# Optimization experiments

Measured on AMD Instinct MI355X. Metric: run time of the kernel, lower is better.

## Reference

```python
import jax, jax.numpy as jnp
import numpy as np

DIM = 2048
N_HEADS = 16
HEAD_DIM = DIM // N_HEADS  # 128
HIDDEN = 8192
EPS = 1e-6
NEG = -1e9


def rmsnorm(x, w):
    xf = x.astype(jnp.float32)
    y = xf * jax.lax.rsqrt(jnp.mean(xf * xf, axis=-1, keepdims=True) + EPS)
    return y.astype(x.dtype) * w


def apply_rope(x, cos, sin):
    # x: [B,S,H,Hd]; cos/sin: [S,Hd//2] -> broadcast [1,S,1,Hd//2]
    xf = x.astype(jnp.float32)
    xr = xf[..., 0::2]
    xi = xf[..., 1::2]
    c = cos[None, :, None, :]
    s = sin[None, :, None, :]
    or_ = xr * c - xi * s
    oi_ = xr * s + xi * c
    out = jnp.stack([or_, oi_], axis=-1).reshape(x.shape)
    return out.astype(x.dtype)


def setup_inputs() -> dict:
    key = jax.random.key(0)
    ks = jax.random.split(key, 10)
    B, S = 1, 2048
    x = jax.random.normal(ks[0], (B, S, DIM), dtype=jnp.float32)
    # RoPE frequencies (Llama-style, theta=10000)
    inv_freq = 1.0 / (10000.0 ** (jnp.arange(0, HEAD_DIM, 2, dtype=jnp.float32) / HEAD_DIM))
    angles = jnp.arange(S, dtype=jnp.float32)[:, None] * inv_freq[None, :]  # [S, Hd//2]
    freqs_cos = jnp.cos(angles)
    freqs_sin = jnp.sin(angles)
    # causal additive mask [1,1,S,S]
    mask = jnp.where(jnp.tril(jnp.ones((S, S), dtype=bool)), 0.0, NEG).astype(jnp.float32)[None, None]
    sc = 0.02
    wq = jax.random.normal(ks[1], (DIM, DIM), dtype=jnp.float32) * sc
    wk = jax.random.normal(ks[2], (DIM, DIM), dtype=jnp.float32) * sc
    wv = jax.random.normal(ks[3], (DIM, DIM), dtype=jnp.float32) * sc
    wo = jax.random.normal(ks[4], (DIM, DIM), dtype=jnp.float32) * sc
    w1 = jax.random.normal(ks[5], (DIM, HIDDEN), dtype=jnp.float32) * sc
    w2 = jax.random.normal(ks[6], (HIDDEN, DIM), dtype=jnp.float32) * sc
    w3 = jax.random.normal(ks[7], (DIM, HIDDEN), dtype=jnp.float32) * sc
    attn_norm_w = jnp.ones((DIM,), dtype=jnp.float32)
    ffn_norm_w = jnp.ones((DIM,), dtype=jnp.float32)
    return {"x": x, "freqs_cos": freqs_cos, "freqs_sin": freqs_sin, "mask": mask,
            "wq": wq, "wk": wk, "wv": wv, "wo": wo, "w1": w1, "w2": w2, "w3": w3,
            "attn_norm_w": attn_norm_w, "ffn_norm_w": ffn_norm_w}


def reference(x, freqs_cos, freqs_sin, mask, wq, wk, wv, wo, w1, w2, w3, attn_norm_w, ffn_norm_w):
    B, S, D = x.shape
    # --- attention (pre-norm) ---
    hn = rmsnorm(x, attn_norm_w)
    q = (hn @ wq).reshape(B, S, N_HEADS, HEAD_DIM)
    k = (hn @ wk).reshape(B, S, N_HEADS, HEAD_DIM)
    v = (hn @ wv).reshape(B, S, N_HEADS, HEAD_DIM)
    q = apply_rope(q, freqs_cos, freqs_sin)
    k = apply_rope(k, freqs_cos, freqs_sin)
    scores = jnp.einsum('bqhd,bkhd->bhqk', q, k) / (HEAD_DIM ** 0.5) + mask
    attn = jax.nn.softmax(scores.astype(jnp.float32), axis=-1).astype(q.dtype)
    ctx = jnp.einsum('bhqk,bkhd->bqhd', attn, v).reshape(B, S, D)
    h = x + ctx @ wo
    # --- SwiGLU FFN (pre-norm) ---
    fn = rmsnorm(h, ffn_norm_w)
    ff = (jax.nn.silu(fn @ w1) * (fn @ w3)) @ w2
    return h + ff
```

## Files before the change

### kernel.cpp

```cpp
#include <hip/hip_runtime.h>
#include <hip/hip_bf16.h>

#define DIM 2048
#define HEAD_DIM 128
#define N_HEADS 16
#define SEQ 2048
#define HID 8192
#define SQKV 6144

typedef short bf16x8 __attribute__((ext_vector_type(8)));
typedef float f32x4 __attribute__((ext_vector_type(4)));
using bf16 = __hip_bfloat16;

#define MFMA16(a, b, c) __builtin_amdgcn_mfma_f32_16x16x32_bf16(a, b, c, 0, 0, 0)

__device__ __forceinline__ unsigned short f2bu(float f) {
    union { bf16 b; unsigned short u; } cv;
    cv.b = __float2bfloat16(f);
    return cv.u;
}

__device__ __forceinline__ void gl16(const void* g, void* l) {
    __builtin_amdgcn_global_load_lds(
        (const __attribute__((address_space(1))) unsigned int*)g,
        (__attribute__((address_space(3))) unsigned int*)l, 16, 0, 0);
}

__global__ __launch_bounds__(256) void rmsnorm_bf16_k(
    const float* __restrict__ x, const float* __restrict__ w, bf16* __restrict__ y)
{
    const int row = blockIdx.x;
    const int tid = threadIdx.x;
    const float* xr = x + (size_t)row * DIM;
    float4 v0 = ((const float4*)xr)[tid];
    float4 v1 = ((const float4*)xr)[tid + 256];
    float ss = v0.x*v0.x + v0.y*v0.y + v0.z*v0.z + v0.w*v0.w
             + v1.x*v1.x + v1.y*v1.y + v1.z*v1.z + v1.w*v1.w;
    for (int o = 32; o > 0; o >>= 1) ss += __shfl_down(ss, o);
    __shared__ float red[4];
    if ((tid & 63) == 0) red[tid >> 6] = ss;
    __syncthreads();
    float tot = red[0] + red[1] + red[2] + red[3];
    float r = rsqrtf(tot * (1.0f / DIM) + 1e-6f);
    float4 w0 = ((const float4*)w)[tid];
    float4 w1 = ((const float4*)w)[tid + 256];
    ushort4 o0, o1;
    o0.x = f2bu(v0.x * r * w0.x); o0.y = f2bu(v0.y * r * w0.y);
    o0.z = f2bu(v0.z * r * w0.z); o0.w = f2bu(v0.w * r * w0.w);
    o1.x = f2bu(v1.x * r * w1.x); o1.y = f2bu(v1.y * r * w1.y);
    o1.z = f2bu(v1.z * r * w1.z); o1.w = f2bu(v1.w * r * w1.w);
    ushort4* yr = (ushort4*)(y + (size_t)row * DIM);
    yr[tid] = o0;
    yr[tid + 256] = o1;
}

__global__ __launch_bounds__(256) void rmsnorm4_k(
    const float* __restrict__ part, const float* __restrict__ x,
    const float* __restrict__ w, float* __restrict__ hout, bf16* __restrict__ y)
{
    const int row = blockIdx.x;
    const int tid = threadIdx.x;
    const size_t base = (size_t)row * DIM;
    const size_t SP = (size_t)SEQ * DIM;
    float4 r0, r1;
    float ss = 0.0f;
    {
        float4 a  = ((const float4*)(x + base))[tid];
        float4 p0 = ((const float4*)(part + base))[tid];
        float4 p1 = ((const float4*)(part + SP + base))[tid];
        float4 p2 = ((const float4*)(part + 2 * SP + base))[tid];
        float4 p3 = ((const float4*)(part + 3 * SP + base))[tid];
        r0.x = a.x + ((p0.x + p1.x) + (p2.x + p3.x));
        r0.y = a.y + ((p0.y + p1.y) + (p2.y + p3.y));
        r0.z = a.z + ((p0.z + p1.z) + (p2.z + p3.z));
        r0.w = a.w + ((p0.w + p1.w) + (p2.w + p3.w));
        ((float4*)(hout + base))[tid] = r0;
        ss += r0.x*r0.x + r0.y*r0.y + r0.z*r0.z + r0.w*r0.w;
    }
    {
        const int t2 = tid + 256;
        float4 a  = ((const float4*)(x + base))[t2];
        float4 p0 = ((const float4*)(part + base))[t2];
        float4 p1 = ((const float4*)(part + SP + base))[t2];
        float4 p2 = ((const float4*)(part + 2 * SP + base))[t2];
        float4 p3 = ((const float4*)(part + 3 * SP + base))[t2];
        r1.x = a.x + ((p0.x + p1.x) + (p2.x + p3.x));
        r1.y = a.y + ((p0.y + p1.y) + (p2.y + p3.y));
        r1.z = a.z + ((p0.z + p1.z) + (p2.z + p3.z));
        r1.w = a.w + ((p0.w + p1.w) + (p2.w + p3.w));
        ((float4*)(hout + base))[t2] = r1;
        ss += r1.x*r1.x + r1.y*r1.y + r1.z*r1.z + r1.w*r1.w;
    }
    for (int o = 32; o > 0; o >>= 1) ss += __shfl_down(ss, o);
    __shared__ float red[4];
    if ((tid & 63) == 0) red[tid >> 6] = ss;
    __syncthreads();
    float tot = red[0] + red[1] + red[2] + red[3];
    float r = rsqrtf(tot * (1.0f / DIM) + 1e-6f);
    float4 w0 = ((const float4*)w)[tid];
    float4 w1 = ((const float4*)w)[tid + 256];
    ushort4 o0, o1;
    o0.x = f2bu(r0.x * r * w0.x); o0.y = f2bu(r0.y * r * w0.y);
    o0.z = f2bu(r0.z * r * w0.z); o0.w = f2bu(r0.w * r * w0.w);
    o1.x = f2bu(r1.x * r * w1.x); o1.y = f2bu(r1.y * r * w1.y);
    o1.z = f2bu(r1.z * r * w1.z); o1.w = f2bu(r1.w * r * w1.w);
    ushort4* yr = (ushort4*)(y + base);
    yr[tid] = o0;
    yr[tid + 256] = o1;
}

__global__ __launch_bounds__(256) void reduce4_k(
    const float* __restrict__ part, const float* __restrict__ h, float* __restrict__ out)
{
    const size_t i = (size_t)blockIdx.x * 256 + threadIdx.x;
    const size_t SP4 = (size_t)SEQ * DIM / 4;
    float4 a  = ((const float4*)h)[i];
    float4 p0 = ((const float4*)part)[i];
    float4 p1 = ((const float4*)part)[i + SP4];
    float4 p2 = ((const float4*)part)[i + 2 * SP4];
    float4 p3 = ((const float4*)part)[i + 3 * SP4];
    float4 r;
    r.x = a.x + ((p0.x + p1.x) + (p2.x + p3.x));
    r.y = a.y + ((p0.y + p1.y) + (p2.y + p3.y));
    r.z = a.z + ((p0.z + p1.z) + (p2.z + p3.z));
    r.w = a.w + ((p0.w + p1.w) + (p2.w + p3.w));
    ((float4*)out)[i] = r;
}

__global__ __launch_bounds__(256) void convT_f32_bf16_k(
    const float* __restrict__ in, bf16* __restrict__ out, int R, int C)
{
    __shared__ float t[32][33];
    const int tx = threadIdx.x, ty = threadIdx.y;
    const int x0 = blockIdx.x * 32, y0 = blockIdx.y * 32;
#pragma unroll
    for (int i = 0; i < 4; ++i)
        t[ty + i * 8][tx] = in[(size_t)(y0 + ty + i * 8) * C + x0 + tx];
    __syncthreads();
#pragma unroll
    for (int i = 0; i < 4; ++i)
        out[(size_t)(x0 + ty + i * 8) * R + y0 + tx] = __float2bfloat16(t[tx][ty + i * 8]);
}

__global__ __launch_bounds__(256) void convT3_f32_bf16_k(
    const float* __restrict__ wq, const float* __restrict__ wk,
    const float* __restrict__ wv, bf16* __restrict__ out)
{
    const int z = blockIdx.z;
    const float* in = z == 0 ? wq : (z == 1 ? wk : wv);
    bf16* o = out + (size_t)z * DIM * DIM;
    __shared__ float t[32][33];
    const int tx = threadIdx.x, ty = threadIdx.y;
    const int x0 = blockIdx.x * 32, y0 = blockIdx.y * 32;
#pragma unroll
    for (int i = 0; i < 4; ++i)
        t[ty + i * 8][tx] = in[(size_t)(y0 + ty + i * 8) * DIM + x0 + tx];
    __syncthreads();
#pragma unroll
    for (int i = 0; i < 4; ++i)
        o[(size_t)(x0 + ty + i * 8) * DIM + y0 + tx] = __float2bfloat16(t[tx][ty + i * 8]);
}

__global__ __launch_bounds__(256) void transpose_bf16_k(
    const bf16* __restrict__ in, int istride, bf16* __restrict__ out)
{
    __shared__ unsigned short t[32][33];
    const int tx = threadIdx.x, ty = threadIdx.y;
    const int x = blockIdx.x * 32 + tx;
    const int y0 = blockIdx.y * 32;
    const unsigned short* inu = (const unsigned short*)in;
    unsigned short* outu = (unsigned short*)out;
#pragma unroll
    for (int i = 0; i < 4; ++i)
        t[ty + i * 8][tx] = inu[(size_t)(y0 + ty + i * 8) * istride + x];
    __syncthreads();
    const int x2 = blockIdx.y * 32 + tx;
    const int y2 = blockIdx.x * 32;
#pragma unroll
    for (int i = 0; i < 4; ++i)
        outu[(size_t)(y2 + ty + i * 8) * SEQ + x2] = t[tx][ty + i * 8];
}

__global__ __launch_bounds__(256) void rope_qk_k(
    bf16* __restrict__ q, bf16* __restrict__ k,
    const float* __restrict__ cosb, const float* __restrict__ sinb)
{
    const int gid = blockIdx.x * 256 + threadIdx.x;
    const int s = gid >> 10;
    const int p = gid & 1023;
    const int h = p >> 6, j = p & 63;
    const size_t off = (size_t)s * SQKV + h * HEAD_DIM + 2 * j;
    const float c = cosb[s * 64 + j], sn = sinb[s * 64 + j];
    float xr = __bfloat162float(q[off]), xi = __bfloat162float(q[off + 1]);
    q[off]     = __float2bfloat16(xr * c - xi * sn);
    q[off + 1] = __float2bfloat16(xr * sn + xi * c);
    xr = __bfloat162float(k[off]); xi = __bfloat162float(k[off + 1]);
    k[off]     = __float2bfloat16(xr * c - xi * sn);
    k[off + 1] = __float2bfloat16(xr * sn + xi * c);
}

template <int EP>
__global__ __launch_bounds__(512, 2) void gemm256_k(
    const bf16* __restrict__ A, const bf16* __restrict__ Bt,
    bf16* __restrict__ Cb, const bf16* other, float* __restrict__ Pf,
    int M, int N, int K, int gx, int ntile, int Ks)
{
    extern __shared__ char smem[];
    const int t512 = threadIdx.x;
    const int w = t512 >> 6, lane = t512 & 63;
    const int lr = lane & 15, lg = lane >> 4;
    const int wm = w >> 2, wn = w & 3;
    const int bofs = (wn & 1) * 64;

    const int nwg = gridDim.x;
    const int q8 = nwg >> 3, r8 = nwg & 7;
    const int xcd = blockIdx.x & 7, seqq = blockIdx.x >> 3;
    const int wgid = (xcd < r8 ? xcd * (q8 + 1) : r8 * (q8 + 1) + (xcd - r8) * q8) + seqq;
    const int split = wgid / ntile;
    const int tile = wgid % ntile;
    const int grp = tile / (4 * gx), rem = tile % (4 * gx);
    const int m0 = (grp * 4 + (rem & 3)) * 256, n0 = (rem >> 2) * 256;
    const int kb0 = split * Ks;
    const int nt = Ks >> 6;

    const bf16* aS[2][2]; const bf16* bS[2][2];
    int sOff[2];
#pragma unroll
    for (int c = 0; c < 2; ++c) {
        const int s = (c * 512 + t512) * 16;
        const int pp = s ^ (((s >> 7) & 7) << 4);
        const int row = pp >> 7, colE = (pp & 127) >> 1;
        sOff[c] = s;
#pragma unroll
        for (int hs = 0; hs < 2; ++hs) {
            aS[hs][c] = A  + (size_t)(m0 + hs * 128 + row) * K + kb0 + colE;
            bS[hs][c] = Bt + (size_t)(n0 + hs * 128 + row) * K + kb0 + colE;
        }
    }
    auto stageA = [&](int buf, int kt) {
#pragma unroll
        for (int hs = 0; hs < 2; ++hs) {
            char* base = smem + (buf * 2 + hs) * 16384;
            gl16(aS[hs][0] + (kt << 6), base + sOff[0]);
            gl16(aS[hs][1] + (kt << 6), base + sOff[1]);
        }
    };
    auto stageB = [&](int buf, int kt) {
#pragma unroll
        for (int hs = 0; hs < 2; ++hs) {
            char* base = smem + 65536 + (buf * 2 + hs) * 16384;
            gl16(bS[hs][0] + (kt << 6), base + sOff[0]);
            gl16(bS[hs][1] + (kt << 6), base + sOff[1]);
        }
    };

    f32x4 acc[8][4] = {};
    bf16x8 bfr[4][2];

    stageB(0, 0); stageA(0, 0);
    stageB(1, 1); stageA(1, 1);

#define SB __builtin_amdgcn_sched_barrier(0)
#define WAITL4 SB; asm volatile("s_waitcnt lgkmcnt(4)" ::: "memory"); SB
#define WAITL0 SB; asm volatile("s_waitcnt lgkmcnt(0)" ::: "memory"); SB
#define LDA_(mf, ks, dst) { int off = (((mf) * 16 + lr) * 128) + ((((ks) * 64) + lg * 16) ^ ((lr & 7) << 4)); \
        dst = *(const bf16x8*)(Am + off); }
#define LDB_(nf, ks, dst) { int off = ((bofs + (nf) * 16 + lr) * 128) + ((((ks) * 64) + lg * 16) ^ ((lr & 7) << 4)); \
        dst = *(const bf16x8*)(Bm + off); }
#define MFMA_PH(mf0, r0, r1, r2, r3) { \
        __builtin_amdgcn_s_setprio(1); \
        _Pragma("unroll") \
        for (int nf = 0; nf < 4; ++nf) { \
            acc[(mf0)][nf]     = MFMA16(r0, bfr[nf][0], acc[(mf0)][nf]); \
            acc[(mf0)][nf]     = MFMA16(r1, bfr[nf][1], acc[(mf0)][nf]); \
            acc[(mf0) + 1][nf] = MFMA16(r2, bfr[nf][0], acc[(mf0) + 1][nf]); \
            acc[(mf0) + 1][nf] = MFMA16(r3, bfr[nf][1], acc[(mf0) + 1][nf]); \
        } \
        __builtin_amdgcn_s_setprio(0); }

    for (int t = 0; t < nt; ++t) {
        const int cur = t & 1;
        if (t + 1 < nt) { asm volatile("s_waitcnt vmcnt(8)" ::: "memory"); }
        else            { asm volatile("s_waitcnt vmcnt(0)" ::: "memory"); }
        SB;
        __builtin_amdgcn_s_barrier();

        const char* Am = smem + (cur * 2 + wm) * 16384;
        const char* Bm = smem + 65536 + (cur * 2 + (wn >> 1)) * 16384;
        const bool pf = (t + 2 < nt);

        bf16x8 x0, x1, x2, x3, y0, y1, y2, y3;
#pragma unroll
        for (int nf = 0; nf < 4; ++nf) { LDB_(nf, 0, bfr[nf][0]) LDB_(nf, 1, bfr[nf][1]) }
        LDA_(0, 0, x0) LDA_(0, 1, x1) LDA_(1, 0, x2) LDA_(1, 1, x3)
        SB;
        LDA_(2, 0, y0) LDA_(2, 1, y1) LDA_(3, 0, y2) LDA_(3, 1, y3)
        WAITL4;
        MFMA_PH(0, x0, x1, x2, x3)
        __builtin_amdgcn_s_barrier();
        if (pf) stageB(cur, t + 2);

        LDA_(4, 0, x0) LDA_(4, 1, x1) LDA_(5, 0, x2) LDA_(5, 1, x3)
        WAITL4;
        MFMA_PH(2, y0, y1, y2, y3)

        LDA_(6, 0, y0) LDA_(6, 1, y1) LDA_(7, 0, y2) LDA_(7, 1, y3)
        WAITL4;
        MFMA_PH(4, x0, x1, x2, x3)

        WAITL0;
        MFMA_PH(6, y0, y1, y2, y3)
        __builtin_amdgcn_s_barrier();
        if (pf) stageA(cur, t + 2);
    }
#undef LDA_
#undef LDB_
#undef MFMA_PH
#undef WAITL4
#undef WAITL0
#undef SB

    float* pf_base = Pf + (size_t)split * M * N;
#pragma unroll
    for (int mf = 0; mf < 8; ++mf)
#pragma unroll
        for (int nf = 0; nf < 4; ++nf) {
            const int row = m0 + wm * 128 + mf * 16 + lg * 4;
            const int col = n0 + wn * 64 + nf * 16 + lr;
#pragma unroll
            for (int r = 0; r < 4; ++r) {
                const size_t idx = (size_t)(row + r) * N + col;
                const float v = acc[mf][nf][r];
                if (EP == 0) {
                    Cb[idx] = __float2bfloat16(v);
                } else if (EP == 2) {
                    const float gg = __bfloat162float(other[idx]);
                    const float sg = gg / (1.0f + __expf(-gg));
                    Cb[idx] = __float2bfloat16(sg * v);
                } else {
                    pf_base[idx] = v;
                }
            }
        }
}

__global__ __launch_bounds__(256) void attn_fwd_k(
    const bf16* __restrict__ qkv, const bf16* __restrict__ vT, bf16* __restrict__ ctx)
{
    const int tid = threadIdx.x;
    const int w = tid >> 6, lane = tid & 63;
    const int lr = lane & 15, lg = lane >> 4;
    const int h = blockIdx.y;
    const int qidx = (blockIdx.y < 8) ? blockIdx.x : (31 - blockIdx.x);
    const int q0b = qidx * 64;
    const int nt = qidx + 1;

    __shared__ __align__(16) unsigned short Kt[2][64 * 128];
    __shared__ __align__(16) unsigned short Vt[2][128 * 64];
    __shared__ __align__(16) unsigned short Pp[4][16 * 64];

    const char* kbase = (const char*)(qkv + DIM + h * HEAD_DIM);
    const char* vbase = (const char*)(vT + (size_t)h * HEAD_DIM * SEQ);

    const int krow_c = tid >> 4;
    const int kcolB  = (tid & 15) * 16;
    const int vrow_c = tid >> 3;
    const int vcolB  = (tid & 7) * 16;

    auto stage = [&](int buf, int kb) {
#pragma unroll
        for (int c = 0; c < 4; ++c) {
            const int r = c * 16 + krow_c;
            gl16(kbase + (size_t)(kb + r) * (SQKV * 2) + (kcolB ^ ((r & 7) << 4)),
                 &Kt[buf][c * 2048 + tid * 8]);
        }
#pragma unroll
        for (int c = 0; c < 4; ++c) {
            const int r = c * 32 + vrow_c;
            gl16(vbase + (size_t)r * (SEQ * 2) + kb * 2 + (vcolB ^ ((r & 7) << 4)),
                 &Vt[buf][c * 2048 + tid * 8]);
        }
    };

    bf16x8 qf[4];
    const bf16* qrow = qkv + (size_t)(q0b + w * 16 + lr) * SQKV + h * HEAD_DIM;
#pragma unroll
    for (int dt = 0; dt < 4; ++dt)
        qf[dt] = *(const bf16x8*)(qrow + dt * 32 + lg * 8);

    f32x4 o[8] = {};
    float m[4], l[4];
#pragma unroll
    for (int j = 0; j < 4; ++j) { m[j] = -3e38f; l[j] = 0.0f; }
    const float scale = 0.08838834764831845f;

    stage(0, 0);
    __syncthreads();

    int cur = 0;
    for (int t = 0; t < nt; ++t) {
        const int kb = t * 64;
        if (t + 1 < nt) stage(cur ^ 1, kb + 64);

        f32x4 s[4] = {};
        __builtin_amdgcn_s_setprio(1);
#pragma unroll
        for (int ss = 0; ss < 4; ++ss) {
            const int r = ss * 16 + lr;
            const int sw = (r & 7) << 3;
#pragma unroll
            for (int dt = 0; dt < 4; ++dt) {
                bf16x8 kf = *(const bf16x8*)&Kt[cur][r * 128 + ((dt * 32 + lg * 8) ^ sw)];
                s[ss] = MFMA16(qf[dt], kf, s[ss]);
            }
        }
        __builtin_amdgcn_s_setprio(0);

        float al[4];
#pragma unroll
        for (int j = 0; j < 4; ++j) {
            const int qi = q0b + w * 16 + lg * 4 + j;
            const int prow = lg * 4 + j;
            const int psw = (prow & 7) << 3;
            float a[4];
#pragma unroll
            for (int ss = 0; ss < 4; ++ss)
                a[ss] = s[ss][j] * scale + ((kb + ss * 16 + lr) > qi ? -1e9f : 0.0f);
            float mx = fmaxf(fmaxf(a[0], a[1]), fmaxf(a[2], a[3]));
            mx = fmaxf(mx, __shfl_xor(mx, 1));
            mx = fmaxf(mx, __shfl_xor(mx, 2));
            mx = fmaxf(mx, __shfl_xor(mx, 4));
            mx = fmaxf(mx, __shfl_xor(mx, 8));
            const float mn = fmaxf(m[j], mx);
            const float asc = __expf(m[j] - mn);
            float e0 = __expf(a[0] - mn), e1 = __expf(a[1] - mn);
            float e2 = __expf(a[2] - mn), e3 = __expf(a[3] - mn);
            float rs = (e0 + e1) + (e2 + e3);
            rs += __shfl_xor(rs, 1); rs += __shfl_xor(rs, 2);
            rs += __shfl_xor(rs, 4); rs += __shfl_xor(rs, 8);
            l[j] = l[j] * asc + rs;
            m[j] = mn;
            al[j] = asc;
            Pp[w][prow * 64 + ((lr)      ^ psw)] = f2bu(e0);
            Pp[w][prow * 64 + ((16 + lr) ^ psw)] = f2bu(e1);
            Pp[w][prow * 64 + ((32 + lr) ^ psw)] = f2bu(e2);
            Pp[w][prow * 64 + ((48 + lr) ^ psw)] = f2bu(e3);
        }
#pragma unroll
        for (int d2 = 0; d2 < 8; ++d2)
#pragma unroll
            for (int j = 0; j < 4; ++j) o[d2][j] *= al[j];

        asm volatile("s_waitcnt lgkmcnt(0)" ::: "memory");
        __builtin_amdgcn_sched_barrier(0);
        const int asw = (lr & 7) << 3;
        bf16x8 pa0 = *(const bf16x8*)&Pp[w][lr * 64 + ((lg * 8)      ^ asw)];
        bf16x8 pa1 = *(const bf16x8*)&Pp[w][lr * 64 + ((32 + lg * 8) ^ asw)];

        __builtin_amdgcn_s_setprio(1);
#pragma unroll
        for (int d2 = 0; d2 < 8; ++d2) {
            const int rv = d2 * 16 + lr;
            const int vsw = (rv & 7) << 3;
            bf16x8 vf0 = *(const bf16x8*)&Vt[cur][rv * 64 + ((lg * 8)      ^ vsw)];
            bf16x8 vf1 = *(const bf16x8*)&Vt[cur][rv * 64 + ((32 + lg * 8) ^ vsw)];
            o[d2] = MFMA16(pa0, vf0, o[d2]);
            o[d2] = MFMA16(pa1, vf1, o[d2]);
        }
        __builtin_amdgcn_s_setprio(0);

        __syncthreads();
        cur ^= 1;
    }

#pragma unroll
    for (int j = 0; j < 4; ++j) {
        const float inv = 1.0f / l[j];
        bf16* dst = ctx + (size_t)(q0b + w * 16 + lg * 4 + j) * DIM + h * HEAD_DIM + lr;
#pragma unroll
        for (int d2 = 0; d2 < 8; ++d2)
            dst[d2 * 16] = __float2bfloat16(o[d2][j] * inv);
    }
}

extern "C" void kernel_launch(void* const* d_in, const int* in_sizes, int n_in,
                              void* d_out, int out_size, void* d_ws, size_t ws_size,
                              hipStream_t stream)
{
    const float* x   = (const float*)d_in[0];
    const float* fc  = (const float*)d_in[1];
    const float* fs  = (const float*)d_in[2];
    const float* wq  = (const float*)d_in[4];
    const float* wk  = (const float*)d_in[5];
    const float* wv  = (const float*)d_in[6];
    const float* wo  = (const float*)d_in[7];
    const float* w1  = (const float*)d_in[8];
    const float* w2  = (const float*)d_in[9];
    const float* w3  = (const float*)d_in[10];
    const float* anw = (const float*)d_in[11];
    const float* fnw = (const float*)d_in[12];
    float* out = (float*)d_out;

    char* p = (char*)d_ws;
    auto alloc = [&](size_t n) { char* r = p; p += (n + 255) & ~(size_t)255; return r; };
    bf16* wT  = (bf16*)alloc((size_t)HID * DIM * 2);
    bf16* hn  = (bf16*)alloc((size_t)SEQ * DIM * 2);
    bf16* qkv = (bf16*)alloc((size_t)SEQ * SQKV * 2);
    bf16* vt  = (bf16*)alloc((size_t)SEQ * DIM * 2);
    bf16* ctx = (bf16*)alloc((size_t)SEQ * DIM * 2);
    bf16* fn  = (bf16*)alloc((size_t)SEQ * DIM * 2);
    float* h  = (float*)alloc((size_t)SEQ * DIM * 4);
    bf16* g   = (bf16*)alloc((size_t)SEQ * HID * 2);
    float* sk = (float*)alloc((size_t)4 * SEQ * DIM * 4);

    const dim3 tb32(32, 8);
    const int LDS256 = 131072;
    (void)hipFuncSetAttribute((const void*)gemm256_k<0>,
        hipFuncAttributeMaxDynamicSharedMemorySize, LDS256);
    (void)hipFuncSetAttribute((const void*)gemm256_k<2>,
        hipFuncAttributeMaxDynamicSharedMemorySize, LDS256);
    (void)hipFuncSetAttribute((const void*)gemm256_k<3>,
        hipFuncAttributeMaxDynamicSharedMemorySize, LDS256);

    rmsnorm_bf16_k<<<SEQ, 256, 0, stream>>>(x, anw, hn);

    convT3_f32_bf16_k<<<dim3(DIM / 32, DIM / 32, 3), tb32, 0, stream>>>(wq, wk, wv, wT);
    gemm256_k<0><<<(SEQ / 256) * (SQKV / 256), 512, LDS256, stream>>>(
        hn, wT, qkv, nullptr, nullptr, SEQ, SQKV, DIM, SQKV / 256, (SEQ / 256) * (SQKV / 256), DIM);

    rope_qk_k<<<(SEQ * 1024) / 256, 256, 0, stream>>>(qkv, qkv + DIM, fc, fs);
    transpose_bf16_k<<<dim3(DIM / 32, SEQ / 32), tb32, 0, stream>>>(qkv + 2 * DIM, SQKV, vt);

    attn_fwd_k<<<dim3(SEQ / 64, N_HEADS), 256, 0, stream>>>(qkv, vt, ctx);

    convT_f32_bf16_k<<<dim3(DIM / 32, DIM / 32), tb32, 0, stream>>>(wo, wT, DIM, DIM);
    gemm256_k<3><<<(SEQ / 256) * (DIM / 256) * 4, 512, LDS256, stream>>>(
        ctx, wT, nullptr, nullptr, sk, SEQ, DIM, DIM, DIM / 256, (SEQ / 256) * (DIM / 256), 512);
    rmsnorm4_k<<<SEQ, 256, 0, stream>>>(sk, x, fnw, h, fn);

    convT_f32_bf16_k<<<dim3(HID / 32, DIM / 32), tb32, 0, stream>>>(w1, wT, DIM, HID);
    gemm256_k<0><<<(SEQ / 256) * (HID / 256), 512, LDS256, stream>>>(
        fn, wT, g, nullptr, nullptr, SEQ, HID, DIM, HID / 256, (SEQ / 256) * (HID / 256), DIM);
    convT_f32_bf16_k<<<dim3(HID / 32, DIM / 32), tb32, 0, stream>>>(w3, wT, DIM, HID);
    gemm256_k<2><<<(SEQ / 256) * (HID / 256), 512, LDS256, stream>>>(
        fn, wT, g, g, nullptr, SEQ, HID, DIM, HID / 256, (SEQ / 256) * (HID / 256), DIM);

    convT_f32_bf16_k<<<dim3(DIM / 32, HID / 32), tb32, 0, stream>>>(w2, wT, HID, DIM);
    gemm256_k<3><<<(SEQ / 256) * (DIM / 256) * 4, 512, LDS256, stream>>>(
        g, wT, nullptr, nullptr, sk, SEQ, DIM, HID, DIM / 256, (SEQ / 256) * (DIM / 256), 2048);
    reduce4_k<<<(SEQ * DIM / 4) / 256, 256, 0, stream>>>(sk, h, out);
}
```

Measured before the change: 514.6 us.

## Restructure GEMM main loop into 8-phase pipeline with fine-grained half-tile staging

Rewrites the 256x256 GEMM main loop to process two K-tiles per iteration in eight phases. Global-to-LDS loads are issued in half-tile pieces between MFMA phases, and each phase is fenced by workgroup barriers. The aim is to spread memory traffic evenly across compute, in the style of ping-pong schedules, so it hides behind MFMA work instead of arriving in bursts. In exchange it adds many more barriers and register reloads of A fragments, and it assumes Ks is a multiple of 128.

```diff
diff --git a/kernel.cpp b/kernel.cpp
--- a/kernel.cpp
+++ b/kernel.cpp
@@ -211,6 +211,7 @@
     const int lr = lane & 15, lg = lane >> 4;
     const int wm = w >> 2, wn = w & 3;
     const int bofs = (wn & 1) * 64;
+    const int swz = (lr & 7) << 4;
 
     const int nwg = gridDim.x;
     const int q8 = nwg >> 3, r8 = nwg & 7;
@@ -221,7 +222,7 @@
     const int grp = tile / (4 * gx), rem = tile % (4 * gx);
     const int m0 = (grp * 4 + (rem & 3)) * 256, n0 = (rem >> 2) * 256;
     const int kb0 = split * Ks;
-    const int nt = Ks >> 6;
+    const int niter = Ks >> 7;
 
     const bf16* aS[2][2]; const bf16* bS[2][2];
     int sOff[2];
@@ -237,88 +238,97 @@
             bS[hs][c] = Bt + (size_t)(n0 + hs * 128 + row) * K + kb0 + colE;
         }
     }
-    auto stageA = [&](int buf, int kt) {
-#pragma unroll
-        for (int hs = 0; hs < 2; ++hs) {
-            char* base = smem + (buf * 2 + hs) * 16384;
-            gl16(aS[hs][0] + (kt << 6), base + sOff[0]);
-            gl16(aS[hs][1] + (kt << 6), base + sOff[1]);
-        }
+    auto stA = [&](int buf, int kt, int hs) {
+        char* base = smem + (buf * 2 + hs) * 16384;
+        gl16(aS[hs][0] + (kt << 6), base + sOff[0]);
+        gl16(aS[hs][1] + (kt << 6), base + sOff[1]);
     };
-    auto stageB = [&](int buf, int kt) {
-#pragma unroll
-        for (int hs = 0; hs < 2; ++hs) {
-            char* base = smem + 65536 + (buf * 2 + hs) * 16384;
-            gl16(bS[hs][0] + (kt << 6), base + sOff[0]);
-            gl16(bS[hs][1] + (kt << 6), base + sOff[1]);
-        }
+    auto stB = [&](int buf, int kt, int hs) {
+        char* base = smem + 65536 + (buf * 2 + hs) * 16384;
+        gl16(bS[hs][0] + (kt << 6), base + sOff[0]);
+        gl16(bS[hs][1] + (kt << 6), base + sOff[1]);
     };
+
+    const char* A0m = smem + (0 * 2 + wm) * 16384;
+    const char* A1m = smem + (1 * 2 + wm) * 16384;
+    const char* B0m = smem + 65536 + (0 * 2 + (wn >> 1)) * 16384;
+    const char* B1m = smem + 65536 + (1 * 2 + (wn >> 1)) * 16384;
 
     f32x4 acc[8][4] = {};
     bf16x8 bfr[4][2];
-
-    stageB(0, 0); stageA(0, 0);
-    stageB(1, 1); stageA(1, 1);
-
-#define SB __builtin_amdgcn_sched_barrier(0)
-#define WAITL4 SB; asm volatile("s_waitcnt lgkmcnt(4)" ::: "memory"); SB
-#define WAITL0 SB; asm volatile("s_waitcnt lgkmcnt(0)" ::: "memory"); SB
-#define LDA_(mf, ks, dst) { int off = (((mf) * 16 + lr) * 128) + ((((ks) * 64) + lg * 16) ^ ((lr & 7) << 4)); \
-        dst = *(const bf16x8*)(Am + off); }
-#define LDB_(nf, ks, dst) { int off = ((bofs + (nf) * 16 + lr) * 128) + ((((ks) * 64) + lg * 16) ^ ((lr & 7) << 4)); \
-        dst = *(const bf16x8*)(Bm + off); }
-#define MFMA_PH(mf0, r0, r1, r2, r3) { \
-        __builtin_amdgcn_s_setprio(1); \
-        _Pragma("unroll") \
-        for (int nf = 0; nf < 4; ++nf) { \
-            acc[(mf0)][nf]     = MFMA16(r0, bfr[nf][0], acc[(mf0)][nf]); \
-            acc[(mf0)][nf]     = MFMA16(r1, bfr[nf][1], acc[(mf0)][nf]); \
-            acc[(mf0) + 1][nf] = MFMA16(r2, bfr[nf][0], acc[(mf0) + 1][nf]); \
-            acc[(mf0) + 1][nf] = MFMA16(r3, bfr[nf][1], acc[(mf0) + 1][nf]); \
-        } \
-        __builtin_amdgcn_s_setprio(0); }
-
-    for (int t = 0; t < nt; ++t) {
-        const int cur = t & 1;
-        if (t + 1 < nt) { asm volatile("s_waitcnt vmcnt(8)" ::: "memory"); }
-        else            { asm volatile("s_waitcnt vmcnt(0)" ::: "memory"); }
-        SB;
-        __builtin_amdgcn_s_barrier();
-
-        const char* Am = smem + (cur * 2 + wm) * 16384;
-        const char* Bm = smem + 65536 + (cur * 2 + (wn >> 1)) * 16384;
-        const bool pf = (t + 2 < nt);
-
-        bf16x8 x0, x1, x2, x3, y0, y1, y2, y3;
-#pragma unroll
-        for (int nf = 0; nf < 4; ++nf) { LDB_(nf, 0, bfr[nf][0]) LDB_(nf, 1, bfr[nf][1]) }
-        LDA_(0, 0, x0) LDA_(0, 1, x1) LDA_(1, 0, x2) LDA_(1, 1, x3)
-        SB;
-        LDA_(2, 0, y0) LDA_(2, 1, y1) LDA_(3, 0, y2) LDA_(3, 1, y3)
-        WAITL4;
-        MFMA_PH(0, x0, x1, x2, x3)
-        __builtin_amdgcn_s_barrier();
-        if (pf) stageB(cur, t + 2);
-
-        LDA_(4, 0, x0) LDA_(4, 1, x1) LDA_(5, 0, x2) LDA_(5, 1, x3)
-        WAITL4;
-        MFMA_PH(2, y0, y1, y2, y3)
-
-        LDA_(6, 0, y0) LDA_(6, 1, y1) LDA_(7, 0, y2) LDA_(7, 1, y3)
-        WAITL4;
-        MFMA_PH(4, x0, x1, x2, x3)
-
-        WAITL0;
-        MFMA_PH(6, y0, y1, y2, y3)
-        __builtin_amdgcn_s_barrier();
-        if (pf) stageA(cur, t + 2);
+    bf16x8 x0, x1, x2, x3;
+
+#define SBAR __builtin_amdgcn_s_barrier()
+#define LGKM0 do { asm volatile("s_waitcnt lgkmcnt(0)" ::: "memory"); \
+                   __builtin_amdgcn_sched_barrier(0); } while (0)
+#define WVM(n) do { asm volatile("s_waitcnt vmcnt(" #n ")" ::: "memory"); \
+                    __builtin_amdgcn_sched_barrier(0); } while (0)
+#define LDA4(base, mf0) do { \
+    x0 = *(const bf16x8*)((base) + (((mf0) * 16 + lr) * 128) + ((lg * 16) ^ swz)); \
+    x1 = *(const bf16x8*)((base) + (((mf0) * 16 + lr) * 128) + ((64 + lg * 16) ^ swz)); \
+    x2 = *(const bf16x8*)((base) + ((((mf0) + 1) * 16 + lr) * 128) + ((lg * 16) ^ swz)); \
+    x3 = *(const bf16x8*)((base) + ((((mf0) + 1) * 16 + lr) * 128) + ((64 + lg * 16) ^ swz)); \
+    } while (0)
+#define LDB8(base) do { \
+    _Pragma("unroll") \
+    for (int nf = 0; nf < 4; ++nf) { \
+        bfr[nf][0] = *(const bf16x8*)((base) + ((bofs + nf * 16 + lr) * 128) + ((lg * 16) ^ swz)); \
+        bfr[nf][1] = *(const bf16x8*)((base) + ((bofs + nf * 16 + lr) * 128) + ((64 + lg * 16) ^ swz)); \
+    } } while (0)
+#define MFMA_PH(mf0) do { \
+    __builtin_amdgcn_s_setprio(1); \
+    _Pragma("unroll") \
+    for (int nf = 0; nf < 4; ++nf) { \
+        acc[(mf0)][nf]     = MFMA16(x0, bfr[nf][0], acc[(mf0)][nf]); \
+        acc[(mf0)][nf]     = MFMA16(x1, bfr[nf][1], acc[(mf0)][nf]); \
+        acc[(mf0) + 1][nf] = MFMA16(x2, bfr[nf][0], acc[(mf0) + 1][nf]); \
+        acc[(mf0) + 1][nf] = MFMA16(x3, bfr[nf][1], acc[(mf0) + 1][nf]); \
+    } \
+    __builtin_amdgcn_s_setprio(0); } while (0)
+
+    stB(0, 0, 0); stB(0, 0, 1); stA(0, 0, 0); stA(0, 0, 1);
+    stB(1, 1, 0); stB(1, 1, 1);
+    WVM(4);
+    SBAR;
+
+    for (int t = 0; t < niter; ++t) {
+        const bool pf = (t + 1 < niter);
+        const int k1 = 2 * t + 1, k2 = 2 * t + 2, k3 = 2 * t + 3;
+
+        stA(1, k1, 0);
+        LDB8(B0m);
+        LDA4(A0m, 0);
+        SBAR; LGKM0; MFMA_PH(0); SBAR;
+        stA(1, k1, 1);
+        LDA4(A0m, 2);
+        SBAR; LGKM0; MFMA_PH(2); SBAR;
+        if (pf) stB(0, k2, 0);
+        LDA4(A0m, 4);
+        SBAR; LGKM0; MFMA_PH(4); SBAR;
+        if (pf) { WVM(2); } else { WVM(0); }
+        if (pf) stB(0, k2, 1);
+        LDA4(A0m, 6);
+        SBAR; LGKM0; MFMA_PH(6); SBAR;
+        if (pf) stA(0, k2, 0);
+        LDB8(B1m);
+        LDA4(A1m, 0);
+        SBAR; LGKM0; MFMA_PH(0); SBAR;
+        if (pf) stA(0, k2, 1);
+        LDA4(A1m, 2);
+        SBAR; LGKM0; MFMA_PH(2); SBAR;
+        if (pf) stB(1, k3, 0);
+        LDA4(A1m, 4);
+        SBAR; LGKM0; MFMA_PH(4); SBAR;
+        if (pf) { WVM(2); stB(1, k3, 1); }
+        LDA4(A1m, 6);
+        SBAR; LGKM0; MFMA_PH(6); SBAR;
     }
-#undef LDA_
-#undef LDB_
+#undef SBAR
+#undef LGKM0
+#undef WVM
+#undef LDA4
+#undef LDB8
 #undef MFMA_PH
-#undef WAITL4
-#undef WAITL0
-#undef SB
 
     float* pf_base = Pf + (size_t)split * M * N;
 #pragma unroll
```

Result: no change. 519.2 us (+0.9%).
